# Optimization experiments

Hardware: AMD Instinct MI355X
Metric: run time of the kernel (lower is better)

Reference implementation:

```python
import jax, jax.numpy as jnp
import numpy as np

L, H, D, DFF, B, S = 4, 8, 512, 2048, 2, 2048
DH = D // H
EPS = 1e-5
SCALE_BASE = 512.0


def setup_inputs() -> dict:
    key = jax.random.key(0)
    ks = jax.random.split(key, 8)
    def w(k, shape, s=0.02):
        return jax.random.normal(k, shape, jnp.float32) * s
    return {
        "x": jax.random.normal(ks[0], (B, S, D), jnp.float32),
        "WQ": w(ks[1], (L, H, D, DH)),
        "WK": w(ks[2], (L, H, D, DH)),
        "WV": w(ks[3], (L, H, D, DH)),
        "WG": w(ks[4], (L, D, D)),
        "WO": w(ks[5], (L, D, D)),
        "gn_w": jnp.ones((L, D), jnp.float32),
        "gn_b": jnp.zeros((L, D), jnp.float32),
        "ln1_w": jnp.ones((L, D), jnp.float32),
        "ln1_b": jnp.zeros((L, D), jnp.float32),
        "ln2_w": jnp.ones((L, D), jnp.float32),
        "ln2_b": jnp.zeros((L, D), jnp.float32),
        "ffn_w1": w(ks[6], (L, D, DFF)),
        "ffn_b1": jnp.zeros((L, DFF), jnp.float32),
        "ffn_w2": w(ks[7], (L, DFF, D)),
        "ffn_b2": jnp.zeros((L, D), jnp.float32),
    }


def _dup(t):
    # duplicate_interleave: [a,b] -> [a,a,b,b]
    return jnp.repeat(t, 2, axis=-1)


def _rot(x):
    # rotate_every_two: (x1,x2) -> (-x2, x1)
    x1, x2 = x[..., ::2], x[..., 1::2]
    return jnp.stack([-x2, x1], axis=-1).reshape(x.shape)


def _xpos(x, downscale):
    # x: [B,H,S,dh]  XPOS rotary with length-extrapolating scale
    s_len, dh = x.shape[-2], x.shape[-1]
    half = dh // 2
    base = (jnp.arange(0, dh, 2, dtype=jnp.float32) + 0.4 * dh) / (1.4 * dh)  # [half]
    power = jnp.arange(s_len, dtype=jnp.float32) / SCALE_BASE
    scale = base[None, :] ** power[:, None]  # [S, half]
    if downscale:
        scale = 1.0 / scale
    inv_freq = 1.0 / (10000.0 ** (jnp.arange(half, dtype=jnp.float32) / half))
    ang = jnp.arange(s_len, dtype=jnp.float32)[:, None] * inv_freq[None, :]
    sin, cos, sc = _dup(jnp.sin(ang)), _dup(jnp.cos(ang)), _dup(scale)
    return x * cos * sc + _rot(x) * sin * sc


def _ln(x, w, b):
    mu = jnp.mean(x, -1, keepdims=True)
    var = jnp.mean((x - mu) ** 2, -1, keepdims=True)
    return (x - mu) * jax.lax.rsqrt(var + EPS) * w + b


def reference(x, WQ, WK, WV, WG, WO, gn_w, gn_b, ln1_w, ln1_b, ln2_w, ln2_b, ffn_w1, ffn_b1, ffn_w2, ffn_b2):
    gammas = 1.0 - jnp.exp(jnp.linspace(np.log(1.0 / 32.0), np.log(1.0 / 512.0), H)).astype(jnp.float32)
    idx = jnp.arange(S, dtype=jnp.float32)
    diff = idx[:, None] - idx[None, :]
    Dmask = jnp.where(diff >= 0, gammas[:, None, None] ** diff, 0.0)  # [H,S,S]
    b = x.shape[0]
    for i in range(L):
        xn = _ln(x, ln1_w[i], ln1_b[i])
        q = _xpos(jnp.einsum('bsd,hde->bhse', xn, WQ[i]), False)
        k = _xpos(jnp.einsum('bsd,hde->bhse', xn, WK[i]), True)
        v = jnp.einsum('bsd,hde->bhse', xn, WV[i])
        att = jnp.einsum('bhse,bhte->bhst', q, k) * Dmask[None]  # [B,H,S,S]
        yh = jnp.einsum('bhst,bhte->bhse', att, v)               # [B,H,S,dh]
        yh = yh.transpose(0, 2, 1, 3)                            # [B,S,H,dh]
        mu = jnp.mean(yh, -1, keepdims=True)
        var = jnp.mean((yh - mu) ** 2, -1, keepdims=True)
        yn = (yh - mu) * jax.lax.rsqrt(var + EPS)
        yn = yn * gn_w[i].reshape(H, DH) + gn_b[i].reshape(H, DH)
        y = yn.reshape(b, S, D)
        g = jax.nn.silu(xn @ WG[i])
        y1 = (g * y) @ WO[i] + x
        h = _ln(y1, ln2_w[i], ln2_b[i])
        x = jax.nn.gelu(h @ ffn_w1[i] + ffn_b1[i], approximate=False) @ ffn_w2[i] + ffn_b2[i] + y1
    return x
```

## Files before the change

kernel.cpp:

```cpp
#include <hip/hip_runtime.h>
#include <hip/hip_bf16.h>

#define LYR 4
#define NH  8
#define DM  512
#define DHD 64
#define DFF 2048
#define BB  2
#define SSL 2048
#define NROWS (BB*SSL)

typedef unsigned short u16;
typedef __attribute__((ext_vector_type(8))) short bf16x8;
typedef __attribute__((ext_vector_type(4))) float f32x4;
typedef __attribute__((ext_vector_type(4))) unsigned int u32x4;

__device__ __forceinline__ u16 f2bf(float f) {
    union { float f; unsigned u; } v; v.f = f;
    unsigned r = v.u + 0x7FFFu + ((v.u >> 16) & 1u);
    return (u16)(r >> 16);
}
__device__ __forceinline__ float bf2f(u16 b) {
    union { unsigned u; float f; } v; v.u = ((unsigned)b) << 16;
    return v.f;
}
__device__ __forceinline__ int swz(int row, int col) {
    return row * 64 + (col & 7) + ((((col >> 3) ^ row) & 7) << 3);
}
__device__ __forceinline__ int swzP(int row, int col) {
    return row * 128 + (col & 7) + ((((col >> 3) ^ row) & 15) << 3);
}
__device__ __forceinline__ void gload16(const u16* g, u16* l) {
    __builtin_amdgcn_global_load_lds(
        (const __attribute__((address_space(1))) unsigned int*)g,
        (__attribute__((address_space(3))) unsigned int*)l, 16, 0, 0);
}
template <int N> __device__ __forceinline__ void wait_vmcnt() {
    if constexpr (N == 0)      asm volatile("s_waitcnt vmcnt(0)" ::: "memory");
    else if constexpr (N == 6) asm volatile("s_waitcnt vmcnt(6)" ::: "memory");
    else static_assert(N == 0 || N == 6, "unsupported vmcnt");
}
__device__ __forceinline__ void block_barrier() {
    __builtin_amdgcn_s_barrier();
    asm volatile("" ::: "memory");
}


__global__ __launch_bounds__(256) void xpos_tables(float4* __restrict__ tab4) {
    const int idx = blockIdx.x * 256 + threadIdx.x;
    const int s = idx >> 5, j = idx & 31;
    const float base = (2.f * j + 0.4f * 64.f) / (1.4f * 64.f);
    const float invf = powf(10000.f, -(float)j / 32.f);
    const float ang = (float)s * invf;
    const float scq = powf(base, (float)s / 512.f);
    tab4[idx] = make_float4(sinf(ang), cosf(ang), scq, 1.f / scq);
}

__global__ __launch_bounds__(256)
void prep_qkv(const float* __restrict__ WQp, const float* __restrict__ WKp,
              const float* __restrict__ WVp, u16* __restrict__ WBT) {
    const int dt = blockIdx.x;
    const int h = blockIdx.y & 7, which = blockIdx.y >> 3;
    const int l = blockIdx.z;
    const float* W = (which == 0 ? WQp : which == 1 ? WKp : WVp);
    const float* ip = W + ((size_t)(l * 8 + h)) * (512 * 64);
    u16* op = WBT + (size_t)l * (2048 * 512) + (size_t)(which * 512 + h * 64) * 512;
    __shared__ u16 tile[64 * 72];
    const int t = threadIdx.x, rr = t >> 2, cc = (t & 3) * 16;
    const float* src = ip + (size_t)(dt * 64 + rr) * 64 + cc;
#pragma unroll
    for (int i = 0; i < 16; ++i) tile[rr * 72 + cc + i] = f2bf(src[i]);
    __syncthreads();
    u16 tmp[16] __attribute__((aligned(16)));
#pragma unroll
    for (int i = 0; i < 16; ++i) tmp[i] = tile[(cc + i) * 72 + rr];
    u16* dst = op + (size_t)rr * 512 + dt * 64 + cc;
    *(u32x4*)&dst[0] = *(const u32x4*)&tmp[0];
    *(u32x4*)&dst[8] = *(const u32x4*)&tmp[8];
}

__global__ __launch_bounds__(256)
void prep_t(const float* __restrict__ in, u16* __restrict__ out, int R, int C,
            long long in_ls, long long out_ls) {
    const float* ip = in + (size_t)blockIdx.z * in_ls;
    u16* op = out + (size_t)blockIdx.z * out_ls;
    const int r0 = blockIdx.x * 64, c0t = blockIdx.y * 64;
    __shared__ u16 tile[64 * 72];
    const int t = threadIdx.x, rr = t >> 2, cc = (t & 3) * 16;
    const float* src = ip + (size_t)(r0 + rr) * C + c0t + cc;
#pragma unroll
    for (int i = 0; i < 16; ++i) tile[rr * 72 + cc + i] = f2bf(src[i]);
    __syncthreads();
    u16 tmp[16] __attribute__((aligned(16)));
#pragma unroll
    for (int i = 0; i < 16; ++i) tmp[i] = tile[(cc + i) * 72 + rr];
    u16* dst = op + (size_t)(c0t + rr) * R + r0 + cc;
    *(u32x4*)&dst[0] = *(const u32x4*)&tmp[0];
    *(u32x4*)&dst[8] = *(const u32x4*)&tmp[8];
}

__global__ __launch_bounds__(256)
void ln_kernel(const float* __restrict__ x, const float* __restrict__ wt,
               const float* __restrict__ bs, u16* __restrict__ out) {
    const int row = blockIdx.x * 4 + (threadIdx.x >> 6);
    const int lane = threadIdx.x & 63;
    const float* xr = x + (size_t)row * DM + lane * 8;
    float v[8];
    *(float4*)&v[0] = *(const float4*)&xr[0];
    *(float4*)&v[4] = *(const float4*)&xr[4];
    float s = 0.f, s2 = 0.f;
#pragma unroll
    for (int i = 0; i < 8; ++i) { s += v[i]; s2 += v[i] * v[i]; }
#pragma unroll
    for (int m = 1; m < 64; m <<= 1) {
        s  += __shfl_xor(s, m, 64);
        s2 += __shfl_xor(s2, m, 64);
    }
    const float mu = s * (1.f / DM);
    const float rs = rsqrtf(s2 * (1.f / DM) - mu * mu + 1e-5f);
    const int e0 = lane * 8;
    u16 o[8] __attribute__((aligned(16)));
#pragma unroll
    for (int i = 0; i < 8; ++i)
        o[i] = f2bf((v[i] - mu) * rs * wt[e0 + i] + bs[e0 + i]);
    *(u32x4*)&out[(size_t)row * DM + e0] = *(const u32x4*)o;
}

template <int BM, int BN, int EPI>
__global__ __launch_bounds__(256)
void gemm_bt(const u16* __restrict__ A, const u16* __restrict__ Bt,
             u16* __restrict__ obf, float* __restrict__ of32,
             const float* __restrict__ res, const float* __restrict__ bias,
             int M, int N, int K) {
    constexpr int FM = BM / 32, FN = BN / 32;
    constexpr int LPS = BM / 32 + BN / 32;
    static_assert(LPS == 6, "vmcnt template expects 6");
    __shared__ __align__(16) u16 As[2][BM * 64];
    __shared__ __align__(16) u16 Bs[2][BN * 64];
    const int t = threadIdx.x;
    const int lane = t & 63, w4 = t >> 6;
    const int wr = w4 >> 1, wc = w4 & 1;
    const int fr = lane & 15, fq = lane >> 4;
    const int nX = N / BN;
    const int nwg = (M / BM) * nX;
    const int swzid = (blockIdx.x & 7) * (nwg >> 3) + (blockIdx.x >> 3);
    const int m0 = (swzid / nX) * BM, n0 = (swzid % nX) * BN;
    const int lr = lane >> 3;
    const int ls = lane & 7;
    const int nsteps = K >> 6;

    auto stage = [&](int step, int slot) {
        const int k0 = step << 6;
#pragma unroll
        for (int q = 0; q < BM / 32; ++q) {
            const int ib = q * 4 + w4;
            const int row = ib * 8 + lr;
            const int cc = ls ^ (row & 7);
            gload16(&A[(size_t)(m0 + row) * K + k0 + cc * 8], &As[slot][ib * 512]);
        }
#pragma unroll
        for (int q = 0; q < BN / 32; ++q) {
            const int ib = q * 4 + w4;
            const int row = ib * 8 + lr;
            const int cc = ls ^ (row & 7);
            gload16(&Bt[(size_t)(n0 + row) * K + k0 + cc * 8], &Bs[slot][ib * 512]);
        }
    };

    f32x4 acc[FM][FN] = {};
    stage(0, 0);
    stage(1, 1);
    for (int st = 0; st < nsteps; ++st) {
        if (st + 1 < nsteps) wait_vmcnt<LPS>(); else wait_vmcnt<0>();
        __builtin_amdgcn_sched_barrier(0);
        block_barrier();
        const u16* Ac = As[st & 1];
        const u16* Bc = Bs[st & 1];
#pragma unroll
        for (int ks = 0; ks < 2; ++ks) {
            bf16x8 av[FM], bv[FN];
#pragma unroll
            for (int i = 0; i < FM; ++i)
                av[i] = *(const bf16x8*)&Ac[swz(wr * (BM / 2) + i * 16 + fr, ks * 32 + fq * 8)];
#pragma unroll
            for (int j = 0; j < FN; ++j)
                bv[j] = *(const bf16x8*)&Bc[swz(wc * (BN / 2) + j * 16 + fr, ks * 32 + fq * 8)];
#pragma unroll
            for (int i = 0; i < FM; ++i)
#pragma unroll
                for (int j = 0; j < FN; ++j)
                    acc[i][j] = __builtin_amdgcn_mfma_f32_16x16x32_bf16(av[i], bv[j], acc[i][j], 0, 0, 0);
        }
        asm volatile("s_waitcnt lgkmcnt(0)" ::: "memory");
        __builtin_amdgcn_sched_barrier(0);
        block_barrier();
        if (st + 2 < nsteps) stage(st + 2, st & 1);
    }
#pragma unroll
    for (int i = 0; i < FM; ++i)
#pragma unroll
        for (int j = 0; j < FN; ++j)
#pragma unroll
            for (int r = 0; r < 4; ++r) {
                const int m = m0 + wr * (BM / 2) + i * 16 + fq * 4 + r;
                const int n = n0 + wc * (BN / 2) + j * 16 + fr;
                const size_t idx = (size_t)m * N + n;
                float v = acc[i][j][r];
                if constexpr (EPI == 1) {
                    of32[idx] = v + res[idx];
                } else {
                    of32[idx] = v + bias[n] + res[idx];
                }
            }
}

template <int EPI>
__global__ __launch_bounds__(512, 1)
void gemm_big(const u16* __restrict__ A, const u16* __restrict__ Bt,
              u16* __restrict__ obf, const float* __restrict__ bias,
              u16* __restrict__ qb, u16* __restrict__ kb, u16* __restrict__ vt,
              u16* __restrict__ gb, const float4* __restrict__ tab4,
              int M, int N, int K) {
    constexpr int BM = 256, BN = 128;
    __shared__ __align__(16) u16 SM[49152];
    const int t = threadIdx.x;
    const int lane = t & 63, w = t >> 6;
    const int wr4 = w >> 1, wc2 = w & 1;
    const int fr = lane & 15, fq = lane >> 4;
    const int nX = N / BN;
    const int nwg = (M / BM) * nX;
    const int swzid = (blockIdx.x & 7) * (nwg >> 3) + (blockIdx.x >> 3);
    const int m0 = (swzid / nX) * BM, n0 = (swzid % nX) * BN;
    const int lr = lane >> 3, ls = lane & 7;
    const int nsteps = K >> 6;

    auto stage = [&](int step, int slot) {
        const int k0 = step << 6;
#pragma unroll
        for (int q = 0; q < 4; ++q) {
            const int ib = q * 8 + w;
            const int row = ib * 8 + lr;
            const int cc = ls ^ (row & 7);
            gload16(&A[(size_t)(m0 + row) * K + k0 + cc * 8], &SM[slot * 16384 + ib * 512]);
        }
#pragma unroll
        for (int q = 0; q < 2; ++q) {
            const int ib = q * 8 + w;
            const int row = ib * 8 + lr;
            const int cc = ls ^ (row & 7);
            gload16(&Bt[(size_t)(n0 + row) * K + k0 + cc * 8],
                    &SM[32768 + slot * 8192 + ib * 512]);
        }
    };

    f32x4 acc[4][4] = {};
    stage(0, 0);
    stage(1, 1);
    for (int st = 0; st < nsteps; ++st) {
        if (st + 1 < nsteps) wait_vmcnt<6>(); else wait_vmcnt<0>();
        __builtin_amdgcn_sched_barrier(0);
        block_barrier();
        const u16* Ac = &SM[(st & 1) * 16384];
        const u16* Bc = &SM[32768 + (st & 1) * 8192];
#pragma unroll
        for (int ks = 0; ks < 2; ++ks) {
            bf16x8 av[4], bv[4];
#pragma unroll
            for (int i = 0; i < 4; ++i)
                av[i] = *(const bf16x8*)&Ac[swz(wr4 * 64 + i * 16 + fr, ks * 32 + fq * 8)];
#pragma unroll
            for (int j = 0; j < 4; ++j)
                bv[j] = *(const bf16x8*)&Bc[swz(wc2 * 64 + j * 16 + fr, ks * 32 + fq * 8)];
            __builtin_amdgcn_s_setprio(1);
#pragma unroll
            for (int i = 0; i < 4; ++i)
#pragma unroll
                for (int j = 0; j < 4; ++j)
                    acc[i][j] = __builtin_amdgcn_mfma_f32_16x16x32_bf16(av[i], bv[j], acc[i][j], 0, 0, 0);
            __builtin_amdgcn_s_setprio(0);
        }
        asm volatile("s_waitcnt lgkmcnt(0)" ::: "memory");
        __builtin_amdgcn_sched_barrier(0);
        block_barrier();
        if (st + 2 < nsteps) stage(st + 2, st & 1);
    }

    if constexpr (EPI == 2) {
#pragma unroll
        for (int i = 0; i < 4; ++i)
#pragma unroll
            for (int j = 0; j < 4; ++j)
#pragma unroll
                for (int r = 0; r < 4; ++r) {
                    const int m = m0 + wr4 * 64 + i * 16 + fq * 4 + r;
                    const int n = n0 + wc2 * 64 + j * 16 + fr;
                    float tt = acc[i][j][r] + bias[n];
                    obf[(size_t)m * N + n] = f2bf(0.5f * tt * (1.f + erff(tt * 0.7071067811865475f)));
                }
    } else {
        const int region = n0 >> 9;
        const int h = (n0 & 511) >> 6;
        const int b = m0 >> 11;
        const int s0 = m0 & 2047;
        if (region == 3) {
#pragma unroll
            for (int i = 0; i < 4; ++i)
#pragma unroll
                for (int j = 0; j < 4; ++j)
#pragma unroll
                    for (int r = 0; r < 4; ++r) {
                        const int m = m0 + wr4 * 64 + i * 16 + fq * 4 + r;
                        const int el = wc2 * 64 + j * 16 + fr;
                        gb[(size_t)m * 512 + (n0 & 511) + el] = f2bf(acc[i][j][r]);
                    }
        } else if (region <= 1) {
            u16* dst = (region == 0) ? qb : kb;
#pragma unroll
            for (int i = 0; i < 4; ++i)
#pragma unroll
                for (int j = 0; j < 4; ++j)
#pragma unroll
                    for (int r = 0; r < 4; ++r) {
                        const int s = s0 + wr4 * 64 + i * 16 + fq * 4 + r;
                        const int el = wc2 * 64 + j * 16 + fr;
                        const int hh = h + (el >> 6), e = el & 63;
                        const float v = acc[i][j][r];
                        const float p = __shfl_xor(v, 1, 64);
                        const float rot = (e & 1) ? p : -p;
                        const float4 t4 = tab4[(size_t)s * 32 + (e >> 1)];
                        const float scl = (region == 0) ? t4.z : t4.w;
                        dst[((size_t)(b * NH + hh) * 2048 + s) * 64 + e] =
                            f2bf((v * t4.y + rot * t4.x) * scl);
                    }
        } else {
            u16* LT = SM;
#pragma unroll
            for (int i = 0; i < 4; ++i)
#pragma unroll
                for (int j = 0; j < 4; ++j)
#pragma unroll
                    for (int r = 0; r < 4; ++r) {
                        const int sl = wr4 * 64 + i * 16 + fq * 4 + r;
                        const int el = wc2 * 64 + j * 16 + fr;
                        LT[el * 264 + sl] = f2bf(acc[i][j][r]);
                    }
            __syncthreads();
            for (int c = t; c < 128 * 32; c += 512) {
                const int er = c >> 5;
                const int sc = (c & 31) * 8;
                const int hh = h + (er >> 6), e = er & 63;
                *(u32x4*)&vt[((size_t)(b * NH + hh) * 64 + e) * 2048 + s0 + sc] =
                    *(const u32x4*)&LT[er * 264 + sc];
            }
        }
    }
}

__global__ __launch_bounds__(512)
void retention(const u16* __restrict__ Qb, const u16* __restrict__ Kb,
               const u16* __restrict__ Vt, const u16* __restrict__ gate,
               const float* __restrict__ gnw, const float* __restrict__ gnb,
               u16* __restrict__ zb) {
    extern __shared__ __align__(16) char smem[];
    u16* KsB = (u16*)smem;
    u16* VsB = (u16*)(smem + 32768);
    u16* Ps  = (u16*)(smem + 65536);

    const int logical = (blockIdx.x & 7) * 64 + (blockIdx.x >> 3);
    const int bh = logical >> 5;
    const int u = logical & 31;
    const int qt = (bh & 1) ? (31 - u) : u;
    const int h = bh & 7, b = bh >> 3;
    const int t = threadIdx.x;
    const int lane = t & 63, w = t >> 6;
    const int fr = lane & 15, fq = lane >> 4;
    const int wr = w & 1, wc2 = w >> 1;
    const int oc = wc2 & 1, th = w >> 2;

    const float gamma = 1.f - expf(-3.4657359f + (float)h * -0.39608410f);
    const float lgam = log2f(gamma);
    const float dlim = 19.931568f / (-lgam);
    const int jt_last = (qt * 64 + 63) >> 7;
    int jt_min = 0;
    {
        const float need = (float)(qt * 64 - 127) - dlim;
        if (need > 0.f) jt_min = (int)ceilf(need * (1.f / 128.f));
        if (jt_min > jt_last) jt_min = jt_last;
        if (jt_min < 0) jt_min = 0;
    }

    float rowf[2][4], colf[2];
#pragma unroll
    for (int i = 0; i < 2; ++i)
#pragma unroll
        for (int rr = 0; rr < 4; ++rr)
            rowf[i][rr] = exp2f((float)(wr * 32 + i * 16 + fq * 4 + rr) * lgam);
#pragma unroll
    for (int j = 0; j < 2; ++j)
        colf[j] = exp2f(-(float)(wc2 * 32 + j * 16 + fr) * lgam);

    const size_t bh2048 = (size_t)bh * 2048;
    const int lr8 = lane >> 3, ls8 = lane & 7;
    const int lr16 = lane >> 4, ls16 = lane & 15;

    bf16x8 qreg[2][2];
#pragma unroll
    for (int i = 0; i < 2; ++i)
#pragma unroll
        for (int ks = 0; ks < 2; ++ks)
            qreg[i][ks] = *(const bf16x8*)&Qb[(bh2048 + qt * 64 + wr * 32 + i * 16 + fr) * 64
                                             + ks * 32 + fq * 8];

    f32x4 oacc[2][2] = {};
    int cur = 0;
    {
        const int jt = jt_min;
        u16* Kd = KsB; u16* Vd = VsB;
#pragma unroll
        for (int q = 0; q < 2; ++q) {
            const int row = q * 64 + w * 8 + lr8;
            const int cc = ls8 ^ (row & 7);
            gload16(&Kb[(bh2048 + jt * 128 + row) * 64 + cc * 8], &Kd[(q * 64 + w * 8) * 64]);
        }
#pragma unroll
        for (int q = 0; q < 2; ++q) {
            const int row = w * 8 + q * 4 + lr16;
            const int cc = ls16 ^ (row & 15);
            gload16(&Vt[((size_t)bh * 64 + row) * 2048 + jt * 128 + cc * 8], &Vd[(w * 8 + q * 4) * 128]);
        }
    }

    for (int jt = jt_min; jt <= jt_last; ++jt) {
        __syncthreads();
        if (jt < jt_last) {
            const int nb = cur ^ 1;
            u16* Kd = KsB + nb * 8192;
            u16* Vd = VsB + nb * 8192;
#pragma unroll
            for (int q = 0; q < 2; ++q) {
                const int row = q * 64 + w * 8 + lr8;
                const int cc = ls8 ^ (row & 7);
                gload16(&Kb[(bh2048 + (jt + 1) * 128 + row) * 64 + cc * 8], &Kd[(q * 64 + w * 8) * 64]);
            }
#pragma unroll
            for (int q = 0; q < 2; ++q) {
                const int row = w * 8 + q * 4 + lr16;
                const int cc = ls16 ^ (row & 15);
                gload16(&Vt[((size_t)bh * 64 + row) * 2048 + (jt + 1) * 128 + cc * 8], &Vd[(w * 8 + q * 4) * 128]);
            }
        }
        const u16* Kc = KsB + cur * 8192;
        f32x4 sac[2][2] = {};
#pragma unroll
        for (int ks = 0; ks < 2; ++ks) {
            bf16x8 kb2[2];
#pragma unroll
            for (int j = 0; j < 2; ++j)
                kb2[j] = *(const bf16x8*)&Kc[swz(wc2 * 32 + j * 16 + fr, ks * 32 + fq * 8)];
#pragma unroll
            for (int i = 0; i < 2; ++i)
#pragma unroll
                for (int j = 0; j < 2; ++j)
                    sac[i][j] = __builtin_amdgcn_mfma_f32_16x16x32_bf16(qreg[i][ks], kb2[j], sac[i][j], 0, 0, 0);
        }
        const float sc = exp2f((float)(qt * 64 - jt * 128) * lgam);
        const bool diag = (jt == jt_last);
#pragma unroll
        for (int i = 0; i < 2; ++i)
#pragma unroll
            for (int j = 0; j < 2; ++j)
#pragma unroll
                for (int rr = 0; rr < 4; ++rr) {
                    float m = sc * rowf[i][rr] * colf[j];
                    if (diag) {
                        const int d = (qt * 64 + wr * 32 + i * 16 + fq * 4 + rr)
                                    - (jt * 128 + wc2 * 32 + j * 16 + fr);
                        if (d < 0) m = 0.f;
                    }
                    Ps[swzP(wr * 32 + i * 16 + fq * 4 + rr, wc2 * 32 + j * 16 + fr)] =
                        f2bf(sac[i][j][rr] * m);
                }
        __syncthreads();
        const u16* Vc = VsB + cur * 8192;
#pragma unroll
        for (int ks = 0; ks < 2; ++ks) {
            const int tcol = th * 64 + ks * 32 + fq * 8;
            bf16x8 pa[2], vb[2];
#pragma unroll
            for (int i = 0; i < 2; ++i)
                pa[i] = *(const bf16x8*)&Ps[swzP(wr * 32 + i * 16 + fr, tcol)];
#pragma unroll
            for (int j = 0; j < 2; ++j)
                vb[j] = *(const bf16x8*)&Vc[swzP(oc * 32 + j * 16 + fr, tcol)];
#pragma unroll
            for (int i = 0; i < 2; ++i)
#pragma unroll
                for (int j = 0; j < 2; ++j)
                    oacc[i][j] = __builtin_amdgcn_mfma_f32_16x16x32_bf16(pa[i], vb[j], oacc[i][j], 0, 0, 0);
        }
        cur ^= 1;
    }

    __syncthreads();
    float* Of = (float*)smem;
    if (th == 1) {
#pragma unroll
        for (int i = 0; i < 2; ++i)
#pragma unroll
            for (int j = 0; j < 2; ++j)
#pragma unroll
                for (int rr = 0; rr < 4; ++rr)
                    Of[(wr * 32 + i * 16 + fq * 4 + rr) * 66 + oc * 32 + j * 16 + fr] = oacc[i][j][rr];
    }
    __syncthreads();
    if (th == 0) {
#pragma unroll
        for (int i = 0; i < 2; ++i)
#pragma unroll
            for (int j = 0; j < 2; ++j)
#pragma unroll
                for (int rr = 0; rr < 4; ++rr) {
                    const int idx = (wr * 32 + i * 16 + fq * 4 + rr) * 66 + oc * 32 + j * 16 + fr;
                    Of[idx] += oacc[i][j][rr];
                }
    }
    __syncthreads();
    const int row = t >> 3, c0 = (t & 7) * 8;
    float v[8];
    float s = 0.f, s2 = 0.f;
#pragma unroll
    for (int i = 0; i < 8; ++i) {
        v[i] = Of[row * 66 + c0 + i];
        s += v[i]; s2 += v[i] * v[i];
    }
    s  += __shfl_xor(s, 1, 64);  s  += __shfl_xor(s, 2, 64);  s  += __shfl_xor(s, 4, 64);
    s2 += __shfl_xor(s2, 1, 64); s2 += __shfl_xor(s2, 2, 64); s2 += __shfl_xor(s2, 4, 64);
    const float mu = s * (1.f / 64.f);
    const float rs = rsqrtf(s2 * (1.f / 64.f) - mu * mu + 1e-5f);
    const int sg = qt * 64 + row;
    u16 gv[8] __attribute__((aligned(16)));
    *(u32x4*)gv = *(const u32x4*)&gate[((size_t)(b * SSL + sg)) * 512 + h * 64 + c0];
    u16 ob[8] __attribute__((aligned(16)));
#pragma unroll
    for (int i = 0; i < 8; ++i) {
        const int dc = h * 64 + c0 + i;
        const float yn = (v[i] - mu) * rs * gnw[dc] + gnb[dc];
        const float g = bf2f(gv[i]);
        ob[i] = f2bf(yn * (g / (1.f + expf(-g))));
    }
    *(u32x4*)&zb[((size_t)(b * SSL + sg)) * 512 + h * 64 + c0] = *(const u32x4*)ob;
}

extern "C" void kernel_launch(void* const* d_in, const int* in_sizes, int n_in,
                              void* d_out, int out_size, void* d_ws, size_t ws_size,
                              hipStream_t stream) {
    const float* X    = (const float*)d_in[0];
    const float* WQ   = (const float*)d_in[1];
    const float* WK   = (const float*)d_in[2];
    const float* WV   = (const float*)d_in[3];
    const float* WG   = (const float*)d_in[4];
    const float* WO   = (const float*)d_in[5];
    const float* GNW  = (const float*)d_in[6];
    const float* GNB  = (const float*)d_in[7];
    const float* LN1W = (const float*)d_in[8];
    const float* LN1B = (const float*)d_in[9];
    const float* LN2W = (const float*)d_in[10];
    const float* LN2B = (const float*)d_in[11];
    const float* FW1  = (const float*)d_in[12];
    const float* FB1  = (const float*)d_in[13];
    const float* FW2  = (const float*)d_in[14];
    const float* FB2  = (const float*)d_in[15];

    char* ws = (char*)d_ws;
    size_t off = 0;
    auto alloc = [&](size_t n) { char* p = ws + off; off += (n + 255) & ~(size_t)255; return p; };

    u16*   WBT  = (u16*)alloc((size_t)LYR * 2048 * 512 * 2);
    u16*   WOT  = (u16*)alloc((size_t)LYR * 512 * 512 * 2);
    u16*   W1T  = (u16*)alloc((size_t)LYR * 2048 * 512 * 2);
    u16*   W2T  = (u16*)alloc((size_t)LYR * 512 * 2048 * 2);
    float4* TAB4 = (float4*)alloc((size_t)2048 * 32 * 16);
    float* XB   = (float*)alloc((size_t)NROWS * DM * 4);
    u16*   XN   = (u16*)alloc((size_t)NROWS * DM * 2);
    u16*   FF1  = (u16*)alloc((size_t)NROWS * 2048 * 2);
    u16*   GB   = (u16*)alloc((size_t)NROWS * DM * 2);
    u16*   QBp  = (u16*)alloc((size_t)NROWS * DM * 2);
    u16*   KBp  = (u16*)alloc((size_t)NROWS * DM * 2);
    u16*   VTp  = (u16*)alloc((size_t)NROWS * DM * 2);
    u16*   ZB   = (u16*)alloc((size_t)NROWS * DM * 2);
    float* Y1   = (float*)alloc((size_t)NROWS * DM * 4);
    u16*   HB   = QBp;

    xpos_tables<<<256, 256, 0, stream>>>(TAB4);
    prep_qkv<<<dim3(8, 24, LYR), 256, 0, stream>>>(WQ, WK, WV, WBT);
    prep_t<<<dim3(8, 8, LYR), 256, 0, stream>>>(WG, WBT + 1536 * 512, 512, 512,
                                                (long long)512 * 512, (long long)2048 * 512);
    prep_t<<<dim3(8, 8, LYR), 256, 0, stream>>>(WO, WOT, 512, 512,
                                                (long long)512 * 512, (long long)512 * 512);
    prep_t<<<dim3(8, 32, LYR), 256, 0, stream>>>(FW1, W1T, 512, 2048,
                                                 (long long)512 * 2048, (long long)2048 * 512);
    prep_t<<<dim3(32, 8, LYR), 256, 0, stream>>>(FW2, W2T, 2048, 512,
                                                 (long long)2048 * 512, (long long)512 * 2048);

    for (int l = 0; l < LYR; ++l) {
        const float* xsrc = (l == 0) ? X : XB;
        float* xdst = (l == LYR - 1) ? (float*)d_out : XB;
        ln_kernel<<<NROWS / 4, 256, 0, stream>>>(xsrc, LN1W + l * 512, LN1B + l * 512, XN);
        gemm_big<4><<<256, 512, 0, stream>>>(
            XN, WBT + (size_t)l * 2048 * 512, nullptr, nullptr,
            QBp, KBp, VTp, GB, TAB4, NROWS, 2048, 512);
        retention<<<512, 512, 81920, stream>>>(QBp, KBp, VTp, GB,
                                               GNW + l * 512, GNB + l * 512, ZB);
        gemm_bt<64, 128, 1><<<256, 256, 0, stream>>>(
            ZB, WOT + (size_t)l * 512 * 512, nullptr, Y1, xsrc, nullptr, NROWS, 512, 512);
        ln_kernel<<<NROWS / 4, 256, 0, stream>>>(Y1, LN2W + l * 512, LN2B + l * 512, HB);
        gemm_big<2><<<256, 512, 0, stream>>>(
            HB, W1T + (size_t)l * 2048 * 512, FF1, FB1 + l * 2048,
            nullptr, nullptr, nullptr, nullptr, nullptr, NROWS, 2048, 512);
        gemm_bt<64, 128, 3><<<256, 256, 0, stream>>>(
            FF1, W2T + (size_t)l * 512 * 2048, nullptr, xdst, Y1, FB2 + l * 512, NROWS, 512, 2048);
    }
}
```

Measured before the change: 461.4 us.

## Replace quadratic retention with chunkwise recurrent form using per-chunk KV states

Replaces the parallel retention kernel, which iterated over all key tiles within the decay window, with a chunkwise formulation. A new intra-chunk kernel computes the masked 64x64 diagonal-block attention and a decay-weighted per-chunk K^T V state. An inter-chunk kernel then sums the decayed prior states (stopping once the decay weight is negligible), applies it to decay-scaled Q, and adds the intra result before group norm and gating. The QKV GEMM epilogue also writes a transposed K copy. This trades repeated QK^T work across long windows for an extra kernel launch, fp32 state and partial-output traffic through global memory (reusing the FF1 buffer), and extra bf16 rounding of the states.

```diff
diff --git a/kernel.cpp b/kernel.cpp
--- a/kernel.cpp
+++ b/kernel.cpp
@@ -26,9 +26,6 @@
 }
 __device__ __forceinline__ int swz(int row, int col) {
     return row * 64 + (col & 7) + ((((col >> 3) ^ row) & 7) << 3);
-}
-__device__ __forceinline__ int swzP(int row, int col) {
-    return row * 128 + (col & 7) + ((((col >> 3) ^ row) & 15) << 3);
 }
 __device__ __forceinline__ void gload16(const u16* g, u16* l) {
     __builtin_amdgcn_global_load_lds(
@@ -218,9 +215,9 @@
 __global__ __launch_bounds__(512, 1)
 void gemm_big(const u16* __restrict__ A, const u16* __restrict__ Bt,
               u16* __restrict__ obf, const float* __restrict__ bias,
-              u16* __restrict__ qb, u16* __restrict__ kb, u16* __restrict__ vt,
-              u16* __restrict__ gb, const float4* __restrict__ tab4,
-              int M, int N, int K) {
+              u16* __restrict__ qb, u16* __restrict__ kb, u16* __restrict__ kt,
+              u16* __restrict__ vt, u16* __restrict__ gb,
+              const float4* __restrict__ tab4, int M, int N, int K) {
     constexpr int BM = 256, BN = 128;
     __shared__ __align__(16) u16 SM[49152];
     const int t = threadIdx.x;
@@ -315,13 +312,15 @@
                     }
         } else if (region <= 1) {
             u16* dst = (region == 0) ? qb : kb;
+            u16* LT = SM;
 #pragma unroll
             for (int i = 0; i < 4; ++i)
 #pragma unroll
                 for (int j = 0; j < 4; ++j)
 #pragma unroll
                     for (int r = 0; r < 4; ++r) {
-                        const int s = s0 + wr4 * 64 + i * 16 + fq * 4 + r;
+                        const int sl = wr4 * 64 + i * 16 + fq * 4 + r;
+                        const int s = s0 + sl;
                         const int el = wc2 * 64 + j * 16 + fr;
                         const int hh = h + (el >> 6), e = el & 63;
                         const float v = acc[i][j][r];
@@ -329,9 +328,20 @@
                         const float rot = (e & 1) ? p : -p;
                         const float4 t4 = tab4[(size_t)s * 32 + (e >> 1)];
                         const float scl = (region == 0) ? t4.z : t4.w;
-                        dst[((size_t)(b * NH + hh) * 2048 + s) * 64 + e] =
-                            f2bf((v * t4.y + rot * t4.x) * scl);
+                        const u16 bv = f2bf((v * t4.y + rot * t4.x) * scl);
+                        dst[((size_t)(b * NH + hh) * 2048 + s) * 64 + e] = bv;
+                        if (region == 1) LT[el * 264 + sl] = bv;
                     }
+            if (region == 1) {
+                __syncthreads();
+                for (int c = t; c < 128 * 32; c += 512) {
+                    const int er = c >> 5;
+                    const int sc = (c & 31) * 8;
+                    const int hh = h + (er >> 6), e = er & 63;
+                    *(u32x4*)&kt[((size_t)(b * NH + hh) * 64 + e) * 2048 + s0 + sc] =
+                        *(const u32x4*)&LT[er * 264 + sc];
+                }
+            }
         } else {
             u16* LT = SM;
 #pragma unroll
@@ -357,187 +367,157 @@
 }
 
 __global__ __launch_bounds__(512)
-void retention(const u16* __restrict__ Qb, const u16* __restrict__ Kb,
-               const u16* __restrict__ Vt, const u16* __restrict__ gate,
+void ret_intra(const u16* __restrict__ Qb, const u16* __restrict__ Kb,
+               const u16* __restrict__ Kt, const u16* __restrict__ Vt,
+               float* __restrict__ OI, float* __restrict__ Tb) {
+    __shared__ __align__(16) u16 Ks[64 * 64];
+    __shared__ __align__(16) u16 KTs[64 * 64];
+    __shared__ __align__(16) u16 Vs[64 * 64];
+    __shared__ __align__(16) u16 Ps[64 * 64];
+    const int logical = (blockIdx.x & 7) * 64 + (blockIdx.x >> 3);
+    const int bh = logical >> 5, n = logical & 31;
+    const int h = bh & 7;
+    const int t = threadIdx.x, lane = t & 63, w = t >> 6;
+    const int fr = lane & 15, fq = lane >> 4;
+    const int wr = w & 1, wc = w >> 1;
+    const float gamma = 1.f - expf(-3.4657359f + (float)h * -0.39608410f);
+    const float lgam = log2f(gamma);
+    const size_t bh2048 = (size_t)bh * 2048;
+    {
+        const int r8 = lane >> 3, g8 = lane & 7;
+        const int row = w * 8 + r8;
+        const int cc = g8 ^ (row & 7);
+        gload16(&Kb[(bh2048 + n * 64 + row) * 64 + cc * 8], &Ks[w * 512]);
+        gload16(&Kt[((size_t)bh * 64 + row) * 2048 + n * 64 + cc * 8], &KTs[w * 512]);
+        gload16(&Vt[((size_t)bh * 64 + row) * 2048 + n * 64 + cc * 8], &Vs[w * 512]);
+    }
+    bf16x8 qa[2][2];
+#pragma unroll
+    for (int i = 0; i < 2; ++i)
+#pragma unroll
+        for (int ks = 0; ks < 2; ++ks)
+            qa[i][ks] = *(const bf16x8*)&Qb[(bh2048 + n * 64 + wr * 32 + i * 16 + fr) * 64
+                                           + ks * 32 + fq * 8];
+    asm volatile("s_waitcnt vmcnt(0)" ::: "memory");
+    block_barrier();
+    f32x4 sac[2] = {};
+#pragma unroll
+    for (int ks = 0; ks < 2; ++ks) {
+        bf16x8 kv = *(const bf16x8*)&Ks[swz(wc * 16 + fr, ks * 32 + fq * 8)];
+#pragma unroll
+        for (int i = 0; i < 2; ++i)
+            sac[i] = __builtin_amdgcn_mfma_f32_16x16x32_bf16(qa[i][ks], kv, sac[i], 0, 0, 0);
+    }
+#pragma unroll
+    for (int i = 0; i < 2; ++i)
+#pragma unroll
+        for (int rr = 0; rr < 4; ++rr) {
+            const int row = wr * 32 + i * 16 + fq * 4 + rr;
+            const int col = wc * 16 + fr;
+            const int d = row - col;
+            const float mval = (d >= 0) ? exp2f(lgam * (float)d) : 0.f;
+            Ps[swz(row, col)] = f2bf(sac[i][rr] * mval);
+        }
+    __syncthreads();
+    f32x4 oacc[2] = {}, tacc[2] = {};
+    const float gi = exp2f(-lgam);
+#pragma unroll
+    for (int ks = 0; ks < 2; ++ks) {
+        bf16x8 vb = *(const bf16x8*)&Vs[swz(wc * 16 + fr, ks * 32 + fq * 8)];
+        bf16x8 ktb = *(const bf16x8*)&KTs[swz(wc * 16 + fr, ks * 32 + fq * 8)];
+#pragma unroll
+        for (int i = 0; i < 2; ++i) {
+            bf16x8 pa = *(const bf16x8*)&Ps[swz(wr * 32 + i * 16 + fr, ks * 32 + fq * 8)];
+            oacc[i] = __builtin_amdgcn_mfma_f32_16x16x32_bf16(pa, vb, oacc[i], 0, 0, 0);
+            bf16x8 vv = *(const bf16x8*)&Vs[swz(wr * 32 + i * 16 + fr, ks * 32 + fq * 8)];
+            bf16x8 vw;
+            float wgt = exp2f(lgam * (float)(64 - ks * 32 - fq * 8));
+#pragma unroll
+            for (int j = 0; j < 8; ++j) {
+                vw[j] = (short)f2bf(bf2f((u16)vv[j]) * wgt);
+                wgt *= gi;
+            }
+            tacc[i] = __builtin_amdgcn_mfma_f32_16x16x32_bf16(vw, ktb, tacc[i], 0, 0, 0);
+        }
+    }
+#pragma unroll
+    for (int i = 0; i < 2; ++i)
+#pragma unroll
+        for (int rr = 0; rr < 4; ++rr) {
+            const int row = wr * 32 + i * 16 + fq * 4 + rr;
+            const int col = wc * 16 + fr;
+            OI[(bh2048 + n * 64 + row) * 64 + col] = oacc[i][rr];
+            Tb[((size_t)(bh * 32 + n)) * 4096 + row * 64 + col] = tacc[i][rr];
+        }
+}
+
+__global__ __launch_bounds__(512)
+void ret_inter(const u16* __restrict__ Qb, const float* __restrict__ Tb,
+               const float* __restrict__ OI, const u16* __restrict__ gate,
                const float* __restrict__ gnw, const float* __restrict__ gnb,
                u16* __restrict__ zb) {
-    extern __shared__ __align__(16) char smem[];
-    u16* KsB = (u16*)smem;
-    u16* VsB = (u16*)(smem + 32768);
-    u16* Ps  = (u16*)(smem + 65536);
-
+    __shared__ __align__(16) u16 Ss[64 * 64];
+    __shared__ float Of[64 * 66];
     const int logical = (blockIdx.x & 7) * 64 + (blockIdx.x >> 3);
-    const int bh = logical >> 5;
-    const int u = logical & 31;
-    const int qt = (bh & 1) ? (31 - u) : u;
+    const int bh = logical >> 5, n = logical & 31;
     const int h = bh & 7, b = bh >> 3;
-    const int t = threadIdx.x;
-    const int lane = t & 63, w = t >> 6;
+    const int t = threadIdx.x, lane = t & 63, w = t >> 6;
     const int fr = lane & 15, fq = lane >> 4;
-    const int wr = w & 1, wc2 = w >> 1;
-    const int oc = wc2 & 1, th = w >> 2;
-
     const float gamma = 1.f - expf(-3.4657359f + (float)h * -0.39608410f);
     const float lgam = log2f(gamma);
-    const float dlim = 19.931568f / (-lgam);
-    const int jt_last = (qt * 64 + 63) >> 7;
-    int jt_min = 0;
+    const size_t bh2048 = (size_t)bh * 2048;
     {
-        const float need = (float)(qt * 64 - 127) - dlim;
-        if (need > 0.f) jt_min = (int)ceilf(need * (1.f / 128.f));
-        if (jt_min > jt_last) jt_min = jt_last;
-        if (jt_min < 0) jt_min = 0;
-    }
-
-    float rowf[2][4], colf[2];
-#pragma unroll
-    for (int i = 0; i < 2; ++i)
-#pragma unroll
-        for (int rr = 0; rr < 4; ++rr)
-            rowf[i][rr] = exp2f((float)(wr * 32 + i * 16 + fq * 4 + rr) * lgam);
-#pragma unroll
-    for (int j = 0; j < 2; ++j)
-        colf[j] = exp2f(-(float)(wc2 * 32 + j * 16 + fr) * lgam);
-
-    const size_t bh2048 = (size_t)bh * 2048;
-    const int lr8 = lane >> 3, ls8 = lane & 7;
-    const int lr16 = lane >> 4, ls16 = lane & 15;
-
-    bf16x8 qreg[2][2];
-#pragma unroll
-    for (int i = 0; i < 2; ++i)
-#pragma unroll
-        for (int ks = 0; ks < 2; ++ks)
-            qreg[i][ks] = *(const bf16x8*)&Qb[(bh2048 + qt * 64 + wr * 32 + i * 16 + fr) * 64
-                                             + ks * 32 + fq * 8];
-
-    f32x4 oacc[2][2] = {};
-    int cur = 0;
-    {
-        const int jt = jt_min;
-        u16* Kd = KsB; u16* Vd = VsB;
-#pragma unroll
-        for (int q = 0; q < 2; ++q) {
-            const int row = q * 64 + w * 8 + lr8;
-            const int cc = ls8 ^ (row & 7);
-            gload16(&Kb[(bh2048 + jt * 128 + row) * 64 + cc * 8], &Kd[(q * 64 + w * 8) * 64]);
-        }
-#pragma unroll
-        for (int q = 0; q < 2; ++q) {
-            const int row = w * 8 + q * 4 + lr16;
-            const int cc = ls16 ^ (row & 15);
-            gload16(&Vt[((size_t)bh * 64 + row) * 2048 + jt * 128 + cc * 8], &Vd[(w * 8 + q * 4) * 128]);
-        }
-    }
-
-    for (int jt = jt_min; jt <= jt_last; ++jt) {
-        __syncthreads();
-        if (jt < jt_last) {
-            const int nb = cur ^ 1;
-            u16* Kd = KsB + nb * 8192;
-            u16* Vd = VsB + nb * 8192;
-#pragma unroll
-            for (int q = 0; q < 2; ++q) {
-                const int row = q * 64 + w * 8 + lr8;
-                const int cc = ls8 ^ (row & 7);
-                gload16(&Kb[(bh2048 + (jt + 1) * 128 + row) * 64 + cc * 8], &Kd[(q * 64 + w * 8) * 64]);
+        const int ev = t >> 3, ek0 = (t & 7) * 8;
+        float sacc[8] = {0.f, 0.f, 0.f, 0.f, 0.f, 0.f, 0.f, 0.f};
+        for (int m = n - 1; m >= 0; --m) {
+            const float wgt = exp2f(lgam * 64.f * (float)(n - 1 - m));
+            if (wgt < 1e-12f) break;
+            const float* src = &Tb[((size_t)(bh * 32 + m)) * 4096 + ev * 64 + ek0];
+#pragma unroll
+            for (int j = 0; j < 8; ++j) sacc[j] += wgt * src[j];
+        }
+#pragma unroll
+        for (int j = 0; j < 8; ++j) Ss[swz(ev, ek0 + j)] = f2bf(sacc[j]);
+    }
+    __syncthreads();
+    f32x4 oacc[2] = {};
+    const int iq = w & 3, j2 = w >> 2;
+    if (n > 0) {
+        const float qs = exp2f(lgam * (float)(iq * 16 + fr));
+#pragma unroll
+        for (int ks = 0; ks < 2; ++ks) {
+            bf16x8 qv = *(const bf16x8*)&Qb[(bh2048 + n * 64 + iq * 16 + fr) * 64
+                                           + ks * 32 + fq * 8];
+            bf16x8 qw;
+#pragma unroll
+            for (int j = 0; j < 8; ++j) qw[j] = (short)f2bf(bf2f((u16)qv[j]) * qs);
+#pragma unroll
+            for (int jj = 0; jj < 2; ++jj) {
+                bf16x8 sv = *(const bf16x8*)&Ss[swz(j2 * 32 + jj * 16 + fr, ks * 32 + fq * 8)];
+                oacc[jj] = __builtin_amdgcn_mfma_f32_16x16x32_bf16(qw, sv, oacc[jj], 0, 0, 0);
             }
-#pragma unroll
-            for (int q = 0; q < 2; ++q) {
-                const int row = w * 8 + q * 4 + lr16;
-                const int cc = ls16 ^ (row & 15);
-                gload16(&Vt[((size_t)bh * 64 + row) * 2048 + (jt + 1) * 128 + cc * 8], &Vd[(w * 8 + q * 4) * 128]);
-            }
-        }
-        const u16* Kc = KsB + cur * 8192;
-        f32x4 sac[2][2] = {};
-#pragma unroll
-        for (int ks = 0; ks < 2; ++ks) {
-            bf16x8 kb2[2];
-#pragma unroll
-            for (int j = 0; j < 2; ++j)
-                kb2[j] = *(const bf16x8*)&Kc[swz(wc2 * 32 + j * 16 + fr, ks * 32 + fq * 8)];
-#pragma unroll
-            for (int i = 0; i < 2; ++i)
-#pragma unroll
-                for (int j = 0; j < 2; ++j)
-                    sac[i][j] = __builtin_amdgcn_mfma_f32_16x16x32_bf16(qreg[i][ks], kb2[j], sac[i][j], 0, 0, 0);
-        }
-        const float sc = exp2f((float)(qt * 64 - jt * 128) * lgam);
-        const bool diag = (jt == jt_last);
-#pragma unroll
-        for (int i = 0; i < 2; ++i)
-#pragma unroll
-            for (int j = 0; j < 2; ++j)
-#pragma unroll
-                for (int rr = 0; rr < 4; ++rr) {
-                    float m = sc * rowf[i][rr] * colf[j];
-                    if (diag) {
-                        const int d = (qt * 64 + wr * 32 + i * 16 + fq * 4 + rr)
-                                    - (jt * 128 + wc2 * 32 + j * 16 + fr);
-                        if (d < 0) m = 0.f;
-                    }
-                    Ps[swzP(wr * 32 + i * 16 + fq * 4 + rr, wc2 * 32 + j * 16 + fr)] =
-                        f2bf(sac[i][j][rr] * m);
-                }
-        __syncthreads();
-        const u16* Vc = VsB + cur * 8192;
-#pragma unroll
-        for (int ks = 0; ks < 2; ++ks) {
-            const int tcol = th * 64 + ks * 32 + fq * 8;
-            bf16x8 pa[2], vb[2];
-#pragma unroll
-            for (int i = 0; i < 2; ++i)
-                pa[i] = *(const bf16x8*)&Ps[swzP(wr * 32 + i * 16 + fr, tcol)];
-#pragma unroll
-            for (int j = 0; j < 2; ++j)
-                vb[j] = *(const bf16x8*)&Vc[swzP(oc * 32 + j * 16 + fr, tcol)];
-#pragma unroll
-            for (int i = 0; i < 2; ++i)
-#pragma unroll
-                for (int j = 0; j < 2; ++j)
-                    oacc[i][j] = __builtin_amdgcn_mfma_f32_16x16x32_bf16(pa[i], vb[j], oacc[i][j], 0, 0, 0);
-        }
-        cur ^= 1;
-    }
-
-    __syncthreads();
-    float* Of = (float*)smem;
-    if (th == 1) {
-#pragma unroll
-        for (int i = 0; i < 2; ++i)
-#pragma unroll
-            for (int j = 0; j < 2; ++j)
-#pragma unroll
-                for (int rr = 0; rr < 4; ++rr)
-                    Of[(wr * 32 + i * 16 + fq * 4 + rr) * 66 + oc * 32 + j * 16 + fr] = oacc[i][j][rr];
-    }
-    __syncthreads();
-    if (th == 0) {
-#pragma unroll
-        for (int i = 0; i < 2; ++i)
-#pragma unroll
-            for (int j = 0; j < 2; ++j)
-#pragma unroll
-                for (int rr = 0; rr < 4; ++rr) {
-                    const int idx = (wr * 32 + i * 16 + fq * 4 + rr) * 66 + oc * 32 + j * 16 + fr;
-                    Of[idx] += oacc[i][j][rr];
-                }
-    }
+        }
+    }
+#pragma unroll
+    for (int jj = 0; jj < 2; ++jj)
+#pragma unroll
+        for (int r = 0; r < 4; ++r)
+            Of[(iq * 16 + fq * 4 + r) * 66 + j2 * 32 + jj * 16 + fr] = oacc[jj][r];
     __syncthreads();
     const int row = t >> 3, c0 = (t & 7) * 8;
     float v[8];
     float s = 0.f, s2 = 0.f;
+    const float* oi = &OI[(bh2048 + n * 64 + row) * 64 + c0];
 #pragma unroll
     for (int i = 0; i < 8; ++i) {
-        v[i] = Of[row * 66 + c0 + i];
+        v[i] = Of[row * 66 + c0 + i] + oi[i];
         s += v[i]; s2 += v[i] * v[i];
     }
     s  += __shfl_xor(s, 1, 64);  s  += __shfl_xor(s, 2, 64);  s  += __shfl_xor(s, 4, 64);
     s2 += __shfl_xor(s2, 1, 64); s2 += __shfl_xor(s2, 2, 64); s2 += __shfl_xor(s2, 4, 64);
     const float mu = s * (1.f / 64.f);
     const float rs = rsqrtf(s2 * (1.f / 64.f) - mu * mu + 1e-5f);
-    const int sg = qt * 64 + row;
+    const int sg = n * 64 + row;
     u16 gv[8] __attribute__((aligned(16)));
     *(u32x4*)gv = *(const u32x4*)&gate[((size_t)(b * SSL + sg)) * 512 + h * 64 + c0];
     u16 ob[8] __attribute__((aligned(16)));
@@ -586,10 +566,13 @@
     u16*   GB   = (u16*)alloc((size_t)NROWS * DM * 2);
     u16*   QBp  = (u16*)alloc((size_t)NROWS * DM * 2);
     u16*   KBp  = (u16*)alloc((size_t)NROWS * DM * 2);
+    u16*   KTp  = (u16*)alloc((size_t)NROWS * DM * 2);
     u16*   VTp  = (u16*)alloc((size_t)NROWS * DM * 2);
     u16*   ZB   = (u16*)alloc((size_t)NROWS * DM * 2);
     float* Y1   = (float*)alloc((size_t)NROWS * DM * 4);
     u16*   HB   = QBp;
+    float* Tb   = (float*)FF1;
+    float* OIb  = (float*)(FF1 + 4194304);
 
     xpos_tables<<<256, 256, 0, stream>>>(TAB4);
     prep_qkv<<<dim3(8, 24, LYR), 256, 0, stream>>>(WQ, WK, WV, WBT);
@@ -608,15 +591,16 @@
         ln_kernel<<<NROWS / 4, 256, 0, stream>>>(xsrc, LN1W + l * 512, LN1B + l * 512, XN);
         gemm_big<4><<<256, 512, 0, stream>>>(
             XN, WBT + (size_t)l * 2048 * 512, nullptr, nullptr,
-            QBp, KBp, VTp, GB, TAB4, NROWS, 2048, 512);
-        retention<<<512, 512, 81920, stream>>>(QBp, KBp, VTp, GB,
-                                               GNW + l * 512, GNB + l * 512, ZB);
+            QBp, KBp, KTp, VTp, GB, TAB4, NROWS, 2048, 512);
+        ret_intra<<<512, 512, 0, stream>>>(QBp, KBp, KTp, VTp, OIb, Tb);
+        ret_inter<<<512, 512, 0, stream>>>(QBp, Tb, OIb, GB,
+                                           GNW + l * 512, GNB + l * 512, ZB);
         gemm_bt<64, 128, 1><<<256, 256, 0, stream>>>(
             ZB, WOT + (size_t)l * 512 * 512, nullptr, Y1, xsrc, nullptr, NROWS, 512, 512);
         ln_kernel<<<NROWS / 4, 256, 0, stream>>>(Y1, LN2W + l * 512, LN2B + l * 512, HB);
         gemm_big<2><<<256, 512, 0, stream>>>(
             HB, W1T + (size_t)l * 2048 * 512, FF1, FB1 + l * 2048,
-            nullptr, nullptr, nullptr, nullptr, nullptr, NROWS, 2048, 512);
+            nullptr, nullptr, nullptr, nullptr, nullptr, nullptr, NROWS, 2048, 512);
         gemm_bt<64, 128, 3><<<256, 256, 0, stream>>>(
             FF1, W2T + (size_t)l * 512 * 2048, nullptr, xdst, Y1, FB2 + l * 512, NROWS, 512, 2048);
     }
```

Result: slower. 482.0 us (+4.5%).

## Triple-buffer GEMM LDS stages, stage Q via LDS, reorder retention tiles

Applied to the files above, without the earlier changes.

Both GEMM kernels move from double to triple LDS buffering. The prefetch of step st+2 is now issued right after the top-of-loop barrier, which removes the second block barrier in each k-step and lets loads overlap more of the MFMA work. The retention kernel now loads its Q tile into LDS and reads it per k-step instead of holding it in registers, which frees registers. Query tiles are also dispatched heaviest-first for every head rather than alternating. The extra LDS in gemm_bt and retention can lower the number of resident blocks per CU.

```diff
diff --git a/kernel.cpp b/kernel.cpp
--- a/kernel.cpp
+++ b/kernel.cpp
@@ -135,8 +135,8 @@
     constexpr int FM = BM / 32, FN = BN / 32;
     constexpr int LPS = BM / 32 + BN / 32;
     static_assert(LPS == 6, "vmcnt template expects 6");
-    __shared__ __align__(16) u16 As[2][BM * 64];
-    __shared__ __align__(16) u16 Bs[2][BN * 64];
+    __shared__ __align__(16) u16 As[3][BM * 64];
+    __shared__ __align__(16) u16 Bs[3][BN * 64];
     const int t = threadIdx.x;
     const int lane = t & 63, w4 = t >> 6;
     const int wr = w4 >> 1, wc = w4 & 1;
@@ -174,8 +174,9 @@
         if (st + 1 < nsteps) wait_vmcnt<LPS>(); else wait_vmcnt<0>();
         __builtin_amdgcn_sched_barrier(0);
         block_barrier();
-        const u16* Ac = As[st & 1];
-        const u16* Bc = Bs[st & 1];
+        if (st + 2 < nsteps) stage(st + 2, (st + 2) % 3);
+        const u16* Ac = As[st % 3];
+        const u16* Bc = Bs[st % 3];
 #pragma unroll
         for (int ks = 0; ks < 2; ++ks) {
             bf16x8 av[FM], bv[FN];
@@ -193,8 +194,6 @@
         }
         asm volatile("s_waitcnt lgkmcnt(0)" ::: "memory");
         __builtin_amdgcn_sched_barrier(0);
-        block_barrier();
-        if (st + 2 < nsteps) stage(st + 2, st & 1);
     }
 #pragma unroll
     for (int i = 0; i < FM; ++i)
@@ -222,7 +221,7 @@
               u16* __restrict__ gb, const float4* __restrict__ tab4,
               int M, int N, int K) {
     constexpr int BM = 256, BN = 128;
-    __shared__ __align__(16) u16 SM[49152];
+    __shared__ __align__(16) u16 SM[73728];
     const int t = threadIdx.x;
     const int lane = t & 63, w = t >> 6;
     const int wr4 = w >> 1, wc2 = w & 1;
@@ -249,7 +248,7 @@
             const int row = ib * 8 + lr;
             const int cc = ls ^ (row & 7);
             gload16(&Bt[(size_t)(n0 + row) * K + k0 + cc * 8],
-                    &SM[32768 + slot * 8192 + ib * 512]);
+                    &SM[49152 + slot * 8192 + ib * 512]);
         }
     };
 
@@ -260,8 +259,9 @@
         if (st + 1 < nsteps) wait_vmcnt<6>(); else wait_vmcnt<0>();
         __builtin_amdgcn_sched_barrier(0);
         block_barrier();
-        const u16* Ac = &SM[(st & 1) * 16384];
-        const u16* Bc = &SM[32768 + (st & 1) * 8192];
+        if (st + 2 < nsteps) stage(st + 2, (st + 2) % 3);
+        const u16* Ac = &SM[(st % 3) * 16384];
+        const u16* Bc = &SM[49152 + (st % 3) * 8192];
 #pragma unroll
         for (int ks = 0; ks < 2; ++ks) {
             bf16x8 av[4], bv[4];
@@ -281,9 +281,8 @@
         }
         asm volatile("s_waitcnt lgkmcnt(0)" ::: "memory");
         __builtin_amdgcn_sched_barrier(0);
-        block_barrier();
-        if (st + 2 < nsteps) stage(st + 2, st & 1);
-    }
+    }
+    block_barrier();
 
     if constexpr (EPI == 2) {
 #pragma unroll
@@ -364,12 +363,12 @@
     extern __shared__ __align__(16) char smem[];
     u16* KsB = (u16*)smem;
     u16* VsB = (u16*)(smem + 32768);
-    u16* Ps  = (u16*)(smem + 65536);
+    u16* Qs  = (u16*)(smem + 65536);
+    u16* Ps  = (u16*)(smem + 73728);
 
     const int logical = (blockIdx.x & 7) * 64 + (blockIdx.x >> 3);
     const int bh = logical >> 5;
-    const int u = logical & 31;
-    const int qt = (bh & 1) ? (31 - u) : u;
+    const int qt = 31 - (logical & 31);
     const int h = bh & 7, b = bh >> 3;
     const int t = threadIdx.x;
     const int lane = t & 63, w = t >> 6;
@@ -403,13 +402,11 @@
     const int lr8 = lane >> 3, ls8 = lane & 7;
     const int lr16 = lane >> 4, ls16 = lane & 15;
 
-    bf16x8 qreg[2][2];
-#pragma unroll
-    for (int i = 0; i < 2; ++i)
-#pragma unroll
-        for (int ks = 0; ks < 2; ++ks)
-            qreg[i][ks] = *(const bf16x8*)&Qb[(bh2048 + qt * 64 + wr * 32 + i * 16 + fr) * 64
-                                             + ks * 32 + fq * 8];
+    {
+        const int row = w * 8 + lr8;
+        const int cc = ls8 ^ (row & 7);
+        gload16(&Qb[(bh2048 + qt * 64 + row) * 64 + cc * 8], &Qs[w * 512]);
+    }
 
     f32x4 oacc[2][2] = {};
     int cur = 0;
@@ -453,7 +450,10 @@
         f32x4 sac[2][2] = {};
 #pragma unroll
         for (int ks = 0; ks < 2; ++ks) {
-            bf16x8 kb2[2];
+            bf16x8 qa[2], kb2[2];
+#pragma unroll
+            for (int i = 0; i < 2; ++i)
+                qa[i] = *(const bf16x8*)&Qs[swz(wr * 32 + i * 16 + fr, ks * 32 + fq * 8)];
 #pragma unroll
             for (int j = 0; j < 2; ++j)
                 kb2[j] = *(const bf16x8*)&Kc[swz(wc2 * 32 + j * 16 + fr, ks * 32 + fq * 8)];
@@ -461,7 +461,7 @@
             for (int i = 0; i < 2; ++i)
 #pragma unroll
                 for (int j = 0; j < 2; ++j)
-                    sac[i][j] = __builtin_amdgcn_mfma_f32_16x16x32_bf16(qreg[i][ks], kb2[j], sac[i][j], 0, 0, 0);
+                    sac[i][j] = __builtin_amdgcn_mfma_f32_16x16x32_bf16(qa[i], kb2[j], sac[i][j], 0, 0, 0);
         }
         const float sc = exp2f((float)(qt * 64 - jt * 128) * lgam);
         const bool diag = (jt == jt_last);
@@ -609,7 +609,7 @@
         gemm_big<4><<<256, 512, 0, stream>>>(
             XN, WBT + (size_t)l * 2048 * 512, nullptr, nullptr,
             QBp, KBp, VTp, GB, TAB4, NROWS, 2048, 512);
-        retention<<<512, 512, 81920, stream>>>(QBp, KBp, VTp, GB,
+        retention<<<512, 512, 90112, stream>>>(QBp, KBp, VTp, GB,
                                                GNW + l * 512, GNB + l * 512, ZB);
         gemm_bt<64, 128, 1><<<256, 256, 0, stream>>>(
             ZB, WOT + (size_t)l * 512 * 512, nullptr, Y1, xsrc, nullptr, NROWS, 512, 512);
```

Measured after the change: 471.6 us. 2.2% more time.
